# Kernel tuning notes

Measured on AMD Instinct MI355X. Metric: run time of the kernel, lower is better.

## Reference

```python
import jax, jax.numpy as jnp
import numpy as np

QMAX = 7.0  # 4-bit symmetric: levels in [-8, 7]

def quant4(w):
    # per-tensor symmetric 4-bit fake-quant with straight-through estimator
    s = jnp.max(jnp.abs(w)) / QMAX
    q = jnp.clip(jnp.round(w / s), -8.0, 7.0) * s
    return w + jax.lax.stop_gradient(q - w)

def setup_inputs() -> dict:
    key = jax.random.key(0)
    ks = jax.random.split(key, 7)
    B = 2048
    x = jax.random.normal(ks[0], (B, 1, 31, 16, 31), dtype=jnp.float32)
    # conv: out_ch=1, in_ch=1, kernel (5,3,5)
    w_conv = jax.random.normal(ks[1], (1, 1, 5, 3, 5), dtype=jnp.float32) * 0.1
    b_conv = jax.random.normal(ks[2], (1,), dtype=jnp.float32) * 0.1
    w_fc1 = jax.random.normal(ks[3], (128, 343), dtype=jnp.float32) * 0.05
    b_fc1 = jax.random.normal(ks[4], (128,), dtype=jnp.float32) * 0.05
    w_fc2 = jax.random.normal(ks[5], (4, 128), dtype=jnp.float32) * 0.05
    b_fc2 = jax.random.normal(ks[6], (4,), dtype=jnp.float32) * 0.05
    return {"x": x, "w_conv": w_conv, "b_conv": b_conv,
            "w_fc1": w_fc1, "b_fc1": b_fc1, "w_fc2": w_fc2, "b_fc2": b_fc2}

def reference(x, w_conv, b_conv, w_fc1, b_fc1, w_fc2, b_fc2):
    # QuantConv3d: 4-bit quantized weights, stride (2,1,2), no padding
    c1 = jax.lax.conv_general_dilated(
        x, quant4(w_conv), window_strides=(2, 1, 2), padding='VALID',
        dimension_numbers=('NCDHW', 'OIDHW', 'NCDHW'))
    c1 = c1 + b_conv.reshape(1, -1, 1, 1, 1)          # [B,1,14,14,14]
    # MaxPool3d(2)
    p1 = jax.lax.reduce_window(c1, -jnp.inf, jax.lax.max,
                               (1, 1, 2, 2, 2), (1, 1, 2, 2, 2), 'VALID')  # [B,1,7,7,7]
    f = p1.reshape(p1.shape[0], -1)                   # [B,343]
    a1 = jax.nn.relu(f @ quant4(w_fc1).T + b_fc1)     # [B,128]
    s2 = a1 @ quant4(w_fc2).T + b_fc2                 # [B,4]
    return jax.nn.softmax(s2, axis=1)
```

## Files before the change

kernel.cpp:

```cpp
#include <hip/hip_runtime.h>

#define WS_WCONV   128
#define WS_W1T     256
#define WS_W2      44160
#define WS_FEAT    45056

__device__ __forceinline__ float q4(float w, float s) {
  if (s <= 0.f) return 0.f;
  float r = rintf(w / s);
  r = fminf(fmaxf(r, -8.f), 7.f);
  return r * s;
}

__global__ __launch_bounds__(256) void quant_all(
    const float* __restrict__ wconv, const float* __restrict__ w1,
    const float* __restrict__ w2, float* __restrict__ ws) {
  __shared__ float red[256];
  int b = blockIdx.x, t = threadIdx.x;
  if (b < 88) {
    const float4* w4 = (const float4*)w1;
    float m = 0.f;
    for (int i = t; i < 10976; i += 256) {
      float4 v = w4[i];
      m = fmaxf(m, fmaxf(fmaxf(fabsf(v.x), fabsf(v.y)),
                         fmaxf(fabsf(v.z), fabsf(v.w))));
    }
    red[t] = m;
    __syncthreads();
    for (int s = 128; s > 0; s >>= 1) {
      if (t < s) red[t] = fmaxf(red[t], red[t + s]);
      __syncthreads();
    }
    float s = red[0] * (1.0f / 7.0f);
    #pragma unroll
    for (int k = 0; k < 2; ++k) {
      int idx = b * 512 + k * 256 + t;
      if (idx < 43904) {
        float q = q4(w1[idx], s);
        int o = idx / 343;
        int j = idx - o * 343;
        ws[WS_W1T + j * 128 + o] = q;
      }
    }
  } else {
    float mc = (t < 75) ? fabsf(wconv[t]) : 0.f;
    float m2 = 0.f;
    for (int i = t; i < 512; i += 256) m2 = fmaxf(m2, fabsf(w2[i]));
    red[t] = mc;
    __syncthreads();
    for (int s = 128; s > 0; s >>= 1) {
      if (t < s) red[t] = fmaxf(red[t], red[t + s]);
      __syncthreads();
    }
    float sc = red[0] * (1.0f / 7.0f);
    __syncthreads();
    red[t] = m2;
    __syncthreads();
    for (int s = 128; s > 0; s >>= 1) {
      if (t < s) red[t] = fmaxf(red[t], red[t + s]);
      __syncthreads();
    }
    float s2 = red[0] * (1.0f / 7.0f);
    if (t < 75) ws[WS_WCONV + t] = q4(wconv[t], sc);
    #pragma unroll
    for (int k = 0; k < 2; ++k) {
      int idx = k * 256 + t;
      ws[WS_W2 + idx] = q4(w2[idx], s2);
    }
  }
}

struct __align__(4) f4u { float x, y, z, w; };

__global__ __launch_bounds__(256, 4) void conv_pool(
    const float* __restrict__ x, const float* __restrict__ bconv,
    const float* __restrict__ ws, float* __restrict__ feat_g) {
  int gid = blockIdx.x * 256 + threadIdx.x;
  int batch = (int)(((unsigned long long)(unsigned)gid * 12521772ull) >> 32);
  int rr = gid - batch * 343;
  int pdl = (rr * 1338) >> 16;
  int r2  = rr - pdl * 49;
  int ph  = (r2 * 9363) >> 16;
  int pw  = r2 - ph * 7;
  const float* wq = ws + WS_WCONV;
  float bc = bconv[0];
  const float* xb = x + (size_t)batch * 15376;
  float c[2][2][2];
  #pragma unroll
  for (int i = 0; i < 8; ++i) ((float*)c)[i] = 0.f;
  const float* b0 = xb + pdl * 1984 + ph * 62 + pw * 4;

  f4u buf[2][4][2];
  #pragma unroll
  for (int hh = 0; hh < 4; ++hh) {
    const float* rp = b0 + hh * 31;
    buf[0][hh][0] = *(const f4u*)rp;
    buf[0][hh][1] = *(const f4u*)(rp + 3);
  }
  #pragma unroll
  for (int dd = 0; dd < 7; ++dd) {
    if (dd < 6) {
      const float* rb = b0 + (dd + 1) * 496;
      #pragma unroll
      for (int hh = 0; hh < 4; ++hh) {
        const float* rp = rb + hh * 31;
        buf[(dd + 1) & 1][hh][0] = *(const f4u*)rp;
        buf[(dd + 1) & 1][hh][1] = *(const f4u*)(rp + 3);
      }
    }
    #pragma unroll
    for (int hh = 0; hh < 4; ++hh) {
      f4u A = buf[dd & 1][hh][0];
      f4u B = buf[dd & 1][hh][1];
      float row[7] = {A.x, A.y, A.z, A.w, B.y, B.z, B.w};
      #pragma unroll
      for (int odp = 0; odp < 2; ++odp) {
        int kd = dd - 2 * odp;
        if (kd < 0 || kd > 4) continue;
        #pragma unroll
        for (int ohp = 0; ohp < 2; ++ohp) {
          int kh = hh - ohp;
          if (kh < 0 || kh > 2) continue;
          #pragma unroll
          for (int owp = 0; owp < 2; ++owp) {
            float a = c[odp][ohp][owp];
            #pragma unroll
            for (int kw = 0; kw < 5; ++kw)
              a = fmaf(row[2 * owp + kw], wq[kd * 15 + kh * 5 + kw], a);
            c[odp][ohp][owp] = a;
          }
        }
      }
    }
  }
  float m = ((float*)c)[0];
  #pragma unroll
  for (int i = 1; i < 8; ++i) m = fmaxf(m, ((float*)c)[i]);
  feat_g[(size_t)batch * 344 + rr] = m + bc;
  if (rr == 0) feat_g[(size_t)batch * 344 + 343] = 0.f;
}

__global__ __launch_bounds__(256) void fc_net(
    const float* __restrict__ ws, const float* __restrict__ bfc1,
    const float* __restrict__ bfc2, float* __restrict__ out) {
  __shared__ alignas(16) float feat[2][344];
  __shared__ float fc1p[2][128];
  __shared__ float a1[2][128];
  __shared__ float s2[2][4];
  int t = threadIdx.x;
  int b0 = blockIdx.x * 2;

  {
    const float4* src = (const float4*)(ws + WS_FEAT + (size_t)b0 * 344);
    float4* dst = (float4*)&feat[0][0];
    if (t < 172) dst[t] = src[t];
  }
  __syncthreads();

  int g = t >> 7, o = t & 127;
  {
    const float* wp = ws + WS_W1T + (g ? 172 * 128 : 0) + o;
    int j0 = g ? 172 : 0;
    float q0[2], q1[2], q2[2], q3[2];
    #pragma unroll
    for (int bb = 0; bb < 2; ++bb) { q0[bb] = q1[bb] = q2[bb] = q3[bb] = 0.f; }
    for (int k = 0; k < 43; ++k) {
      float w0 = wp[0], w1 = wp[128], w2 = wp[256], w3 = wp[384];
      #pragma unroll
      for (int bb = 0; bb < 2; ++bb) {
        float4 ff = *(const float4*)&feat[bb][j0 + k * 4];
        q0[bb] = fmaf(ff.x, w0, q0[bb]);
        q1[bb] = fmaf(ff.y, w1, q1[bb]);
        q2[bb] = fmaf(ff.z, w2, q2[bb]);
        q3[bb] = fmaf(ff.w, w3, q3[bb]);
      }
      wp += 512;
    }
    #pragma unroll
    for (int bb = 0; bb < 2; ++bb) {
      float acc = (q0[bb] + q1[bb]) + (q2[bb] + q3[bb]);
      if (g) fc1p[bb][o] = acc;
      else   a1[bb][o] = acc;
    }
    __syncthreads();
    #pragma unroll
    for (int bb = 0; bb < 2; ++bb)
      if (!g) a1[bb][o] = fmaxf(a1[bb][o] + fc1p[bb][o] + bfc1[o], 0.f);
  }
  __syncthreads();

  if (t < 128) {
    int w = t >> 6, l = t & 63;
    int cls = l & 3, kk = l >> 2;
    const float* w2p = ws + WS_W2 + cls * 128 + kk * 8;
    const float* av = &a1[w][kk * 8];
    float p = 0.f;
    #pragma unroll
    for (int i = 0; i < 8; ++i) p = fmaf(av[i], w2p[i], p);
    p += __shfl_down(p, 32);
    p += __shfl_down(p, 16);
    p += __shfl_down(p, 8);
    p += __shfl_down(p, 4);
    if (l < 4) s2[w][l] = p + bfc2[l];
  }
  __syncthreads();
  if (t < 8) {
    int w = t >> 2, cls = t & 3;
    float v0 = s2[w][0], v1 = s2[w][1], v2 = s2[w][2], v3 = s2[w][3];
    float m = fmaxf(fmaxf(v0, v1), fmaxf(v2, v3));
    float e0 = expf(v0 - m), e1 = expf(v1 - m);
    float e2 = expf(v2 - m), e3 = expf(v3 - m);
    float inv = 1.f / (e0 + e1 + e2 + e3);
    float mine = (cls == 0) ? e0 : (cls == 1) ? e1 : (cls == 2) ? e2 : e3;
    out[(b0 + w) * 4 + cls] = mine * inv;
  }
}

extern "C" void kernel_launch(void* const* d_in, const int* in_sizes, int n_in,
                              void* d_out, int out_size, void* d_ws, size_t ws_size,
                              hipStream_t stream) {
  const float* x     = (const float*)d_in[0];
  const float* wconv = (const float*)d_in[1];
  const float* bconv = (const float*)d_in[2];
  const float* wfc1  = (const float*)d_in[3];
  const float* bfc1  = (const float*)d_in[4];
  const float* wfc2  = (const float*)d_in[5];
  const float* bfc2  = (const float*)d_in[6];
  float* out = (float*)d_out;
  float* ws  = (float*)d_ws;

  quant_all<<<89, 256, 0, stream>>>(wconv, wfc1, wfc2, ws);
  conv_pool<<<2744, 256, 0, stream>>>(x, bconv, ws, ws + WS_FEAT);
  fc_net<<<1024, 256, 0, stream>>>(ws, bfc1, bfc2, out);
}
```

Measured before the change: 228.2 us.

## Compute up to 2x2 pooled outputs per thread in conv_pool to reuse input rows

Each conv_pool thread now produces a 2x2 block of pooled (h,w) outputs instead of one. Rows shared by neighbouring h outputs are loaded once per column pass, so fewer global loads are issued and the batch/index decode is done once per four outputs. The grid shrinks from 2744 to 896 blocks. The cost is more registers and accumulators per thread, fewer threads and waves to hide latency, and a partially idle thread wherever a 2x2 block overhangs the 7x7 edge.

```diff
diff --git a/kernel.cpp b/kernel.cpp
--- a/kernel.cpp
+++ b/kernel.cpp
@@ -72,72 +72,83 @@
 
 struct __align__(4) f4u { float x, y, z, w; };
 
+__device__ __forceinline__ void conv_2ph(
+    const float* __restrict__ bcol,
+    const float* __restrict__ wq, bool i1ok, float bc,
+    float* __restrict__ fcol) {
+  float c[2][2][2][2];
+  #pragma unroll
+  for (int k = 0; k < 16; ++k) ((float*)c)[k] = 0.f;
+  #pragma unroll
+  for (int dd = 0; dd < 7; ++dd) {
+    const float* rb = bcol + dd * 496;
+    #pragma unroll
+    for (int hg = 0; hg < 6; ++hg) {
+      if (hg >= 4 && !i1ok) continue;
+      const float* rp = rb + hg * 31;
+      f4u A = *(const f4u*)rp;
+      f4u B = *(const f4u*)(rp + 3);
+      float row[7] = {A.x, A.y, A.z, A.w, B.y, B.z, B.w};
+      #pragma unroll
+      for (int i = 0; i < 2; ++i) {
+        int hh = hg - 2 * i;
+        if (hh < 0 || hh > 3) continue;
+        #pragma unroll
+        for (int odp = 0; odp < 2; ++odp) {
+          int kd = dd - 2 * odp;
+          if (kd < 0 || kd > 4) continue;
+          #pragma unroll
+          for (int ohp = 0; ohp < 2; ++ohp) {
+            int kh = hh - ohp;
+            if (kh < 0 || kh > 2) continue;
+            #pragma unroll
+            for (int owp = 0; owp < 2; ++owp) {
+              float a = c[i][odp][ohp][owp];
+              #pragma unroll
+              for (int kw = 0; kw < 5; ++kw)
+                a = fmaf(row[2 * owp + kw], wq[kd * 15 + kh * 5 + kw], a);
+              c[i][odp][ohp][owp] = a;
+            }
+          }
+        }
+      }
+    }
+  }
+  #pragma unroll
+  for (int i = 0; i < 2; ++i) {
+    if (i == 1 && !i1ok) continue;
+    float m = c[i][0][0][0];
+    m = fmaxf(m, c[i][0][0][1]);
+    m = fmaxf(m, c[i][0][1][0]);
+    m = fmaxf(m, c[i][0][1][1]);
+    m = fmaxf(m, c[i][1][0][0]);
+    m = fmaxf(m, c[i][1][0][1]);
+    m = fmaxf(m, c[i][1][1][0]);
+    m = fmaxf(m, c[i][1][1][1]);
+    fcol[i * 7] = m + bc;
+  }
+}
+
 __global__ __launch_bounds__(256, 4) void conv_pool(
     const float* __restrict__ x, const float* __restrict__ bconv,
     const float* __restrict__ ws, float* __restrict__ feat_g) {
   int gid = blockIdx.x * 256 + threadIdx.x;
-  int batch = (int)(((unsigned long long)(unsigned)gid * 12521772ull) >> 32);
-  int rr = gid - batch * 343;
-  int pdl = (rr * 1338) >> 16;
-  int r2  = rr - pdl * 49;
-  int ph  = (r2 * 9363) >> 16;
-  int pw  = r2 - ph * 7;
+  int batch = (int)(((unsigned long long)(unsigned)gid * 38347923ull) >> 32);
+  int rem = gid - batch * 112;
+  int pd  = rem >> 4;
+  int phb = (rem >> 2) & 3;
+  int pwb = rem & 3;
+  int ph0 = phb * 2, pw0 = pwb * 2;
+  bool i1ok = (phb < 3), j1ok = (pwb < 3);
   const float* wq = ws + WS_WCONV;
   float bc = bconv[0];
-  const float* xb = x + (size_t)batch * 15376;
-  float c[2][2][2];
-  #pragma unroll
-  for (int i = 0; i < 8; ++i) ((float*)c)[i] = 0.f;
-  const float* b0 = xb + pdl * 1984 + ph * 62 + pw * 4;
-
-  f4u buf[2][4][2];
-  #pragma unroll
-  for (int hh = 0; hh < 4; ++hh) {
-    const float* rp = b0 + hh * 31;
-    buf[0][hh][0] = *(const f4u*)rp;
-    buf[0][hh][1] = *(const f4u*)(rp + 3);
-  }
-  #pragma unroll
-  for (int dd = 0; dd < 7; ++dd) {
-    if (dd < 6) {
-      const float* rb = b0 + (dd + 1) * 496;
-      #pragma unroll
-      for (int hh = 0; hh < 4; ++hh) {
-        const float* rp = rb + hh * 31;
-        buf[(dd + 1) & 1][hh][0] = *(const f4u*)rp;
-        buf[(dd + 1) & 1][hh][1] = *(const f4u*)(rp + 3);
-      }
-    }
-    #pragma unroll
-    for (int hh = 0; hh < 4; ++hh) {
-      f4u A = buf[dd & 1][hh][0];
-      f4u B = buf[dd & 1][hh][1];
-      float row[7] = {A.x, A.y, A.z, A.w, B.y, B.z, B.w};
-      #pragma unroll
-      for (int odp = 0; odp < 2; ++odp) {
-        int kd = dd - 2 * odp;
-        if (kd < 0 || kd > 4) continue;
-        #pragma unroll
-        for (int ohp = 0; ohp < 2; ++ohp) {
-          int kh = hh - ohp;
-          if (kh < 0 || kh > 2) continue;
-          #pragma unroll
-          for (int owp = 0; owp < 2; ++owp) {
-            float a = c[odp][ohp][owp];
-            #pragma unroll
-            for (int kw = 0; kw < 5; ++kw)
-              a = fmaf(row[2 * owp + kw], wq[kd * 15 + kh * 5 + kw], a);
-            c[odp][ohp][owp] = a;
-          }
-        }
-      }
-    }
-  }
-  float m = ((float*)c)[0];
-  #pragma unroll
-  for (int i = 1; i < 8; ++i) m = fmaxf(m, ((float*)c)[i]);
-  feat_g[(size_t)batch * 344 + rr] = m + bc;
-  if (rr == 0) feat_g[(size_t)batch * 344 + 343] = 0.f;
+  const float* xb = x + (size_t)batch * 15376 + pd * 1984 + ph0 * 62;
+  float* fb = feat_g + (size_t)batch * 344 + pd * 49 + ph0 * 7;
+
+  conv_2ph(xb + pw0 * 4, wq, i1ok, bc, fb + pw0);
+  if (j1ok)
+    conv_2ph(xb + pw0 * 4 + 4, wq, i1ok, bc, fb + pw0 + 1);
+  if (rem == 0) feat_g[(size_t)batch * 344 + 343] = 0.f;
 }
 
 __global__ __launch_bounds__(256) void fc_net(
@@ -230,6 +241,6 @@
   float* ws  = (float*)d_ws;
 
   quant_all<<<89, 256, 0, stream>>>(wconv, wfc1, wfc2, ws);
-  conv_pool<<<2744, 256, 0, stream>>>(x, bconv, ws, ws + WS_FEAT);
+  conv_pool<<<896, 256, 0, stream>>>(x, bconv, ws, ws + WS_FEAT);
   fc_net<<<1024, 256, 0, stream>>>(ws, bfc1, bfc2, out);
 }
```

After: 362.0 us. 1.59x slower.
